# Kernel tuning notes

Measured on AMD Instinct MI355X. Metric: run time of the kernel, lower is better.

Reference implementation:

```python
import jax, jax.numpy as jnp
import numpy as np

K = 16  # neighbors
EPS = 1e-3  # Keras BatchNormalization default epsilon


def _bn(x, gamma, beta, mean, var):
    return (x - mean) * jax.lax.rsqrt(var + EPS) * gamma + beta


def setup_inputs() -> dict:
    key = jax.random.key(0)
    ks = jax.random.split(key, 16)
    B, P, C = 128, 256, 64
    inp = {
        "points": jax.random.normal(ks[0], (B, P, 3), jnp.float32),
        "features": jax.random.normal(ks[1], (B, P, C), jnp.float32),
        "w0": jax.random.normal(ks[2], (2 * C, 64), jnp.float32) * 0.08,
        "w1": jax.random.normal(ks[3], (64, 64), jnp.float32) * 0.12,
        "w2": jax.random.normal(ks[4], (64, 64), jnp.float32) * 0.12,
        "gammas": 0.8 + 0.4 * jax.random.uniform(ks[5], (3, 64), jnp.float32),
        "betas": 0.1 * jax.random.normal(ks[6], (3, 64), jnp.float32),
        "means": 0.1 * jax.random.normal(ks[7], (3, 64), jnp.float32),
        "variances": 0.5 + jax.random.uniform(ks[8], (3, 64), jnp.float32),
        "sc_w": jax.random.normal(ks[9], (C, 64), jnp.float32) * 0.12,
        "sc_gamma": 0.8 + 0.4 * jax.random.uniform(ks[10], (64,), jnp.float32),
        "sc_beta": 0.1 * jax.random.normal(ks[11], (64,), jnp.float32),
        "sc_mean": 0.1 * jax.random.normal(ks[12], (64,), jnp.float32),
        "sc_var": 0.5 + jax.random.uniform(ks[13], (64,), jnp.float32),
    }
    return inp


def reference(points, features, w0, w1, w2, gammas, betas, means, variances,
              sc_w, sc_gamma, sc_beta, sc_mean, sc_var):
    B, P, C = features.shape
    # pairwise squared-distance matrix: ||a||^2 - 2 a.b + ||b||^2  -> [B, P, P]
    r = jnp.sum(points * points, axis=2, keepdims=True)  # [B, P, 1]
    m = jnp.einsum('bpc,bqc->bpq', points, points)
    d = r - 2.0 * m + jnp.swapaxes(r, 1, 2)
    # top_k of -d: K+1 nearest (incl. self at position 0), drop self
    _, idx = jax.lax.top_k(-d, K + 1)
    idx = idx[:, :, 1:]  # [B, P, K]
    # KNN gather of features
    knn_fts = features[jnp.arange(B)[:, None, None], idx]  # [B, P, K, C]
    center = jnp.broadcast_to(features[:, :, None, :], (B, P, K, C))
    x = jnp.concatenate([center, knn_fts - center], axis=-1)  # [B, P, K, 2C]
    # per-edge MLP: 1x1 conv + BN (inference) + relu
    for i, w in enumerate((w0, w1, w2)):
        x = jnp.einsum('bpkc,cd->bpkd', x, w)
        x = _bn(x, gammas[i], betas[i], means[i], variances[i])
        x = jax.nn.relu(x)
    fts = jnp.mean(x, axis=2)  # average pooling over neighbors -> [B, P, 64]
    # shortcut 1x1 conv + BN
    sc = jnp.einsum('bpc,cd->bpd', features, sc_w)
    sc = _bn(sc, sc_gamma, sc_beta, sc_mean, sc_var)
    return jax.nn.relu(sc + fts)
```

## Files before the change

### kernel.cpp

```cpp
#include <hip/hip_runtime.h>
#include <math.h>

#define NBATCH 128
#define NP 256
#define NC 64
#define KNN 16
#define EPSV 1e-3f

typedef __bf16 bf16_t;
typedef bf16_t bf16x8 __attribute__((ext_vector_type(8)));
typedef float f32x4 __attribute__((ext_vector_type(4)));
typedef unsigned short u16x4 __attribute__((ext_vector_type(4)));

static __device__ __forceinline__ f32x4 mfma16(bf16x8 a, bf16x8 b, f32x4 c) {
    return __builtin_amdgcn_mfma_f32_16x16x32_bf16(a, b, c, 0, 0, 0);
}
static __device__ __forceinline__ unsigned short f2bfu(float f) {
    union { bf16_t b; unsigned short u; } cv; cv.b = (bf16_t)f; return cv.u;
}
static __device__ __forceinline__ float bfu2f(unsigned short u) {
    unsigned x = ((unsigned)u) << 16;
    return __int_as_float((int)x);
}
static __device__ __forceinline__ unsigned umin2(unsigned a, unsigned b) { return a < b ? a : b; }
static __device__ __forceinline__ unsigned umax2(unsigned a, unsigned b) { return a > b ? a : b; }

static __device__ __forceinline__ bf16x8 packrelu(f32x4 a, f32x4 b) {
    bf16x8 r;
    r[0] = (bf16_t)fmaxf(a[0], 0.f); r[1] = (bf16_t)fmaxf(a[1], 0.f);
    r[2] = (bf16_t)fmaxf(a[2], 0.f); r[3] = (bf16_t)fmaxf(a[3], 0.f);
    r[4] = (bf16_t)fmaxf(b[0], 0.f); r[5] = (bf16_t)fmaxf(b[1], 0.f);
    r[6] = (bf16_t)fmaxf(b[2], 0.f); r[7] = (bf16_t)fmaxf(b[3], 0.f);
    return r;
}

template <int CTRL>
static __device__ __forceinline__ float dppadd(float v) {
    int x = __builtin_amdgcn_mov_dpp(__float_as_int(v), CTRL, 0xF, 0xF, true);
    return v + __int_as_float(x);
}
static __device__ __forceinline__ float sum16(float v) {
    v = dppadd<0xB1>(v);
    v = dppadd<0x4E>(v);
    v = dppadd<0x141>(v);
    v = dppadd<0x140>(v);
    return v;
}

#define CFENCE() asm volatile("" ::: "memory")

#define INSERTK(k_)                                                   \
    do {                                                              \
        _Pragma("unroll")                                             \
        for (int ii = KNN - 1; ii >= 1; --ii)                         \
            bk[ii] = umin2(umax2((k_), bk[ii - 1]), bk[ii]);          \
        bk[0] = umin2((k_), bk[0]);                                   \
    } while (0)

__global__ __launch_bounds__(256) void prep_kernel(
    const float* __restrict__ w0, const float* __restrict__ w1,
    const float* __restrict__ w2, const float* __restrict__ sc_w,
    const float* __restrict__ gammas, const float* __restrict__ betas,
    const float* __restrict__ means, const float* __restrict__ variances,
    const float* __restrict__ sc_gamma, const float* __restrict__ sc_beta,
    const float* __restrict__ sc_mean, const float* __restrict__ sc_var,
    unsigned short* __restrict__ wsf, float* __restrict__ bnp)
{
    const int tid = blockIdx.x * 256 + threadIdx.x;
    if (tid < 20480) {
        const int region = tid >> 12;
        const int e2 = tid & 4095;
        const int f = e2 >> 9;
        const int r = e2 & 511;
        const int lane = r >> 3, j = r & 7;
        const int ks = f >> 2, t = f & 3;
        const int m = lane & 15;
        const int k_in = ks * 32 + (lane >> 4) * 8 + j;
        const int kp = (t >> 1) * 32 + (m >> 2) * 8 + (t & 1) * 4 + (m & 3);
        float v;
        if (region == 0)      v = w0[k_in * 64 + kp] - w0[(64 + k_in) * 64 + kp];
        else if (region == 1) v = w0[(64 + k_in) * 64 + kp];
        else if (region == 2) {
            float s1 = gammas[k_in] * rsqrtf(variances[k_in] + EPSV);
            v = s1 * w1[k_in * 64 + kp];
        } else if (region == 3) {
            float s2 = gammas[64 + k_in] * rsqrtf(variances[64 + k_in] + EPSV);
            v = s2 * w2[k_in * 64 + kp];
        } else {
            v = sc_w[k_in * 64 + (4 * m + t)];
        }
        wsf[tid] = f2bfu(v);
    } else {
        const int e = tid - 20480;
        if (e < 192) {
            const int L = e >> 6;
            const int pos = e & 63;
            const int t = pos >> 4, m = pos & 15;
            const int c = (t >> 1) * 32 + (m >> 2) * 8 + (t & 1) * 4 + (m & 3);
            float scl = gammas[L * 64 + c] * rsqrtf(variances[L * 64 + c] + EPSV);
            float shf = betas[L * 64 + c] - means[L * 64 + c] * scl;
            bnp[e] = shf / scl;
        } else if (e < 256) {
            const int c = e - 192;
            float s3 = gammas[128 + c] * rsqrtf(variances[128 + c] + EPSV);
            bnp[e] = s3 * (1.f / 16.f);
        } else if (e < 320) {
            const int c = e - 256;
            bnp[e] = sc_gamma[c] * rsqrtf(sc_var[c] + EPSV);
        } else if (e < 384) {
            const int c = e - 320;
            float s = sc_gamma[c] * rsqrtf(sc_var[c] + EPSV);
            bnp[e] = sc_beta[c] - sc_mean[c] * s;
        }
    }
}

__global__ __launch_bounds__(256) void mega_kernel(
    const float* __restrict__ points, const float* __restrict__ features,
    const unsigned short* __restrict__ wsf, const float* __restrict__ bnp,
    float* __restrict__ out)
{
    __shared__ __align__(16) unsigned short fLDS[NP * NC];
    __shared__ __align__(16) float4 sp[NP];
    __shared__ unsigned sk[128][17];
    __shared__ unsigned short nkbuf[128][16];
    __shared__ __align__(16) float s0buf[4][8][64];
    __shared__ __align__(16) unsigned short ftsbuf[4][8][64];

    const int kb = blockIdx.x;
    const int bb = kb >> 1;
    const int qbase = (kb & 1) * 128;
    const int t = threadIdx.x;

    {
        const float* pb = points + (size_t)bb * NP * 3;
        sp[t] = make_float4(pb[t * 3 + 0], pb[t * 3 + 1], pb[t * 3 + 2], 0.f);
        const float* fb = features + (size_t)bb * NP * NC;
#pragma unroll
        for (int cc = 0; cc < 8; ++cc) {
            const int c = t + cc * 256;
            const int row = c >> 3, ch8 = c & 7;
            const float4 a = *(const float4*)&fb[row * NC + ch8 * 8];
            const float4 b2 = *(const float4*)&fb[row * NC + ch8 * 8 + 4];
            union { unsigned short s[8]; uint4 v; } r;
            r.s[0] = f2bfu(a.x); r.s[1] = f2bfu(a.y); r.s[2] = f2bfu(a.z); r.s[3] = f2bfu(a.w);
            r.s[4] = f2bfu(b2.x); r.s[5] = f2bfu(b2.y); r.s[6] = f2bfu(b2.z); r.s[7] = f2bfu(b2.w);
            const int sc = ch8 ^ (row & 7);
            *(uint4*)&fLDS[row * NC + sc * 8] = r.v;
        }
    }
    __syncthreads();

    {
        const int qt = t & 127;
        const int half = t >> 7;
        const int p = qbase + qt;
        const float4 qp = sp[p];
        unsigned bk[KNN];
#pragma unroll
        for (int ii = 0; ii < KNN; ++ii) bk[ii] = 0xFFFFFFFFu;
        const int cbase = half * 128;
#pragma unroll 4
        for (int c = 0; c < 128; ++c) {
            const int cand = cbase + c;
            const float4 P = sp[cand];
            const float dx = qp.x - P.x, dy = qp.y - P.y, dz = qp.z - P.z;
            const float d = fmaf(dx, dx, fmaf(dy, dy, dz * dz));
            unsigned key = (__float_as_uint(d) & 0xFFFFFF00u) | (unsigned)cand;
            key = (cand == p) ? 0xFFFFFFFFu : key;
            INSERTK(key);
        }
        if (half == 1) {
#pragma unroll
            for (int ii = 0; ii < KNN; ++ii) sk[qt][ii] = bk[ii];
        }
        __syncthreads();
        if (half == 0) {
            for (int j = 0; j < KNN; ++j) {
                const unsigned key = sk[qt][j];
                if (key >= bk[KNN - 1]) break;
                INSERTK(key);
            }
#pragma unroll
            for (int ii = 0; ii < KNN; ++ii)
                nkbuf[qt][ii] = (unsigned short)(bk[ii] & 0xFFu);
        }
    }
    __syncthreads();

    const int wid = t >> 6;
    const int l = t & 63;
    const int i = l & 15;
    const int h = l >> 4;

    bf16x8 wr[24];
    {
        const bf16x8* __restrict__ W = (const bf16x8*)(wsf + 4096);
#pragma unroll
        for (int f = 0; f < 24; ++f) wr[f] = W[f * 64 + l];
    }
    f32x4 cin2[4], cin3[4];
#pragma unroll
    for (int tq = 0; tq < 4; ++tq) {
        cin2[tq] = *(const f32x4*)&bnp[64 + tq * 16 + 4 * h];
        cin3[tq] = *(const f32x4*)&bnp[128 + tq * 16 + 4 * h];
    }

    const bf16x8* __restrict__ WV = (const bf16x8*)(wsf);
    const bf16x8* __restrict__ WS = (const bf16x8*)(wsf + 16384);

    for (int seg = 0; seg < 4; ++seg) {
        const int qr0 = seg * 32 + wid * 8;

        {
            const int crow = qbase + qr0 + (i & 7);
            const int swl = crow & 7;
            bf16x8 b0 = *(const bf16x8*)&fLDS[crow * NC + (h ^ swl) * 8];
            bf16x8 b1 = *(const bf16x8*)&fLDS[crow * NC + ((4 + h) ^ swl) * 8];
#pragma unroll
            for (int tq = 0; tq < 4; ++tq) {
                f32x4 acc = *(const f32x4*)&bnp[tq * 16 + 4 * h];
                acc = mfma16(WV[tq * 64 + l], b0, acc);
                acc = mfma16(WV[(4 + tq) * 64 + l], b1, acc);
                if (i < 8)
                    *(f32x4*)&s0buf[wid][i][tq * 16 + 4 * h] = acc;
            }
        }
        int nks[8];
#pragma unroll
        for (int q = 0; q < 8; ++q) nks[q] = nkbuf[qr0 + q][i];
        CFENCE();

        bf16x8 fb0, fb1;
        {
            const int nk = nks[0], swn = nk & 7;
            fb0 = *(const bf16x8*)&fLDS[nk * NC + (h ^ swn) * 8];
            fb1 = *(const bf16x8*)&fLDS[nk * NC + ((4 + h) ^ swn) * 8];
        }

#pragma unroll
        for (int q = 0; q < 8; ++q) {
            f32x4 acc[4];
#pragma unroll
            for (int tq = 0; tq < 4; ++tq) {
                f32x4 z = *(const f32x4*)&s0buf[wid][q][tq * 16 + 4 * h];
                z = mfma16(wr[tq], fb0, z);
                acc[tq] = mfma16(wr[4 + tq], fb1, z);
            }
            bf16x8 g0, g1;
            if (q < 7) {
                const int nk = nks[q + 1], swn = nk & 7;
                g0 = *(const bf16x8*)&fLDS[nk * NC + (h ^ swn) * 8];
                g1 = *(const bf16x8*)&fLDS[nk * NC + ((4 + h) ^ swn) * 8];
            }
            bf16x8 x0 = packrelu(acc[0], acc[1]);
            bf16x8 x1 = packrelu(acc[2], acc[3]);
#pragma unroll
            for (int tq = 0; tq < 4; ++tq) {
                f32x4 z = mfma16(wr[8 + tq], x0, cin2[tq]);
                acc[tq] = mfma16(wr[12 + tq], x1, z);
            }
            bf16x8 y0 = packrelu(acc[0], acc[1]);
            bf16x8 y1 = packrelu(acc[2], acc[3]);
#pragma unroll
            for (int tq = 0; tq < 4; ++tq) {
                f32x4 z = mfma16(wr[16 + tq], y0, cin3[tq]);
                acc[tq] = mfma16(wr[20 + tq], y1, z);
            }
            float st[4][4];
#pragma unroll
            for (int tq = 0; tq < 4; ++tq)
#pragma unroll
                for (int r = 0; r < 4; ++r)
                    st[tq][r] = sum16(fmaxf(acc[tq][r], 0.f));
            if (i == 0) {
#pragma unroll
                for (int tq = 0; tq < 4; ++tq) {
                    u16x4 pk;
#pragma unroll
                    for (int r = 0; r < 4; ++r) pk[r] = f2bfu(st[tq][r]);
                    *(u16x4*)&ftsbuf[wid][q][(tq >> 1) * 32 + h * 8 + (tq & 1) * 4] = pk;
                }
            }
            fb0 = g0; fb1 = g1;
        }
        CFENCE();

        {
            const int i4 = 4 * i;
            float4 sscl = *(const float4*)&bnp[256 + i4];
            float4 sshf = *(const float4*)&bnp[320 + i4];
            float4 f3q  = *(const float4*)&bnp[192 + i4];
            const int crow = qbase + qr0 + (i & 7);
            const int swl = crow & 7;
            bf16x8 a0 = *(const bf16x8*)&fLDS[crow * NC + (h ^ swl) * 8];
            bf16x8 a1 = *(const bf16x8*)&fLDS[crow * NC + ((4 + h) ^ swl) * 8];
            f32x4 acc[4];
#pragma unroll
            for (int tq = 0; tq < 4; ++tq) {
                f32x4 z = {0.f, 0.f, 0.f, 0.f};
                z = mfma16(a0, WS[tq * 64 + l], z);
                acc[tq] = mfma16(a1, WS[(4 + tq) * 64 + l], z);
            }
            if (h < 2) {
                const float* ss_ = (const float*)&sscl;
                const float* sf_ = (const float*)&sshf;
                const float* f3_ = (const float*)&f3q;
#pragma unroll
                for (int r = 0; r < 4; ++r) {
                    const int q = h * 4 + r;
                    u16x4 ftsu = *(const u16x4*)&ftsbuf[wid][q][i4];
                    float4 o;
                    float* o_ = (float*)&o;
#pragma unroll
                    for (int tq = 0; tq < 4; ++tq)
                        o_[tq] = fmaxf(fmaf(acc[tq][r], ss_[tq], sf_[tq]) + bfu2f(ftsu[tq]) * f3_[tq], 0.f);
                    *(float4*)&out[(size_t)(bb * NP + qbase + qr0 + q) * NC + i4] = o;
                }
            }
        }
        CFENCE();
    }
}

extern "C" void kernel_launch(void* const* d_in, const int* in_sizes, int n_in,
                              void* d_out, int out_size, void* d_ws, size_t ws_size,
                              hipStream_t stream) {
    const float* points    = (const float*)d_in[0];
    const float* features  = (const float*)d_in[1];
    const float* w0        = (const float*)d_in[2];
    const float* w1        = (const float*)d_in[3];
    const float* w2        = (const float*)d_in[4];
    const float* gammas    = (const float*)d_in[5];
    const float* betas     = (const float*)d_in[6];
    const float* means     = (const float*)d_in[7];
    const float* variances = (const float*)d_in[8];
    const float* sc_w      = (const float*)d_in[9];
    const float* sc_gamma  = (const float*)d_in[10];
    const float* sc_beta   = (const float*)d_in[11];
    const float* sc_mean   = (const float*)d_in[12];
    const float* sc_var    = (const float*)d_in[13];
    float* out = (float*)d_out;

    unsigned short* wsf = (unsigned short*)d_ws;
    float* bnp = (float*)((char*)d_ws + 40960);

    prep_kernel<<<82, 256, 0, stream>>>(w0, w1, w2, sc_w, gammas, betas, means,
                                        variances, sc_gamma, sc_beta, sc_mean,
                                        sc_var, wsf, bnp);
    mega_kernel<<<NBATCH * 2, 256, 0, stream>>>(points, features, wsf, bnp, out);
}
```

Measured before the change: 51.80 us.

## Split work into 32-query blocks with tree KNN merge and direct global gathers

Result: slower. 54.76 us (+5.7%).

```diff
diff --git a/kernel.cpp b/kernel.cpp
--- a/kernel.cpp
+++ b/kernel.cpp
@@ -25,6 +25,12 @@
 static __device__ __forceinline__ unsigned umin2(unsigned a, unsigned b) { return a < b ? a : b; }
 static __device__ __forceinline__ unsigned umax2(unsigned a, unsigned b) { return a > b ? a : b; }
 
+static __device__ __forceinline__ bf16x8 pack8(float4 a, float4 b) {
+    bf16x8 r;
+    r[0] = (bf16_t)a.x; r[1] = (bf16_t)a.y; r[2] = (bf16_t)a.z; r[3] = (bf16_t)a.w;
+    r[4] = (bf16_t)b.x; r[5] = (bf16_t)b.y; r[6] = (bf16_t)b.z; r[7] = (bf16_t)b.w;
+    return r;
+}
 static __device__ __forceinline__ bf16x8 packrelu(f32x4 a, f32x4 b) {
     bf16x8 r;
     r[0] = (bf16_t)fmaxf(a[0], 0.f); r[1] = (bf16_t)fmaxf(a[1], 0.f);
@@ -115,53 +121,41 @@
     }
 }
 
-__global__ __launch_bounds__(256) void mega_kernel(
+__global__ __launch_bounds__(256) void knedge_kernel(
     const float* __restrict__ points, const float* __restrict__ features,
     const unsigned short* __restrict__ wsf, const float* __restrict__ bnp,
     float* __restrict__ out)
 {
-    __shared__ __align__(16) unsigned short fLDS[NP * NC];
     __shared__ __align__(16) float4 sp[NP];
-    __shared__ unsigned sk[128][17];
-    __shared__ unsigned short nkbuf[128][16];
+    __shared__ unsigned mrg[32][4][17];
+    __shared__ unsigned short nkbuf[32][16];
     __shared__ __align__(16) float s0buf[4][8][64];
     __shared__ __align__(16) unsigned short ftsbuf[4][8][64];
-
-    const int kb = blockIdx.x;
-    const int bb = kb >> 1;
-    const int qbase = (kb & 1) * 128;
+    __shared__ __align__(16) float cinlds[128];
+
+    const int kb = (blockIdx.x & 7) * 128 + (blockIdx.x >> 3);
+    const int bb = kb >> 3;
+    const int q0 = (kb & 7) * 32;
     const int t = threadIdx.x;
 
     {
         const float* pb = points + (size_t)bb * NP * 3;
         sp[t] = make_float4(pb[t * 3 + 0], pb[t * 3 + 1], pb[t * 3 + 2], 0.f);
-        const float* fb = features + (size_t)bb * NP * NC;
-#pragma unroll
-        for (int cc = 0; cc < 8; ++cc) {
-            const int c = t + cc * 256;
-            const int row = c >> 3, ch8 = c & 7;
-            const float4 a = *(const float4*)&fb[row * NC + ch8 * 8];
-            const float4 b2 = *(const float4*)&fb[row * NC + ch8 * 8 + 4];
-            union { unsigned short s[8]; uint4 v; } r;
-            r.s[0] = f2bfu(a.x); r.s[1] = f2bfu(a.y); r.s[2] = f2bfu(a.z); r.s[3] = f2bfu(a.w);
-            r.s[4] = f2bfu(b2.x); r.s[5] = f2bfu(b2.y); r.s[6] = f2bfu(b2.z); r.s[7] = f2bfu(b2.w);
-            const int sc = ch8 ^ (row & 7);
-            *(uint4*)&fLDS[row * NC + sc * 8] = r.v;
-        }
+        if (t < 128) cinlds[t] = bnp[64 + t];
     }
     __syncthreads();
 
     {
-        const int qt = t & 127;
-        const int half = t >> 7;
-        const int p = qbase + qt;
+        const int q = t & 31;
+        const int oct = t >> 5;
+        const int p = q0 + q;
         const float4 qp = sp[p];
         unsigned bk[KNN];
 #pragma unroll
         for (int ii = 0; ii < KNN; ++ii) bk[ii] = 0xFFFFFFFFu;
-        const int cbase = half * 128;
+        const int cbase = oct * 32;
 #pragma unroll 4
-        for (int c = 0; c < 128; ++c) {
+        for (int c = 0; c < 32; ++c) {
             const int cand = cbase + c;
             const float4 P = sp[cand];
             const float dx = qp.x - P.x, dy = qp.y - P.y, dz = qp.z - P.z;
@@ -170,20 +164,49 @@
             key = (cand == p) ? 0xFFFFFFFFu : key;
             INSERTK(key);
         }
-        if (half == 1) {
-#pragma unroll
-            for (int ii = 0; ii < KNN; ++ii) sk[qt][ii] = bk[ii];
-        }
-        __syncthreads();
-        if (half == 0) {
+        if (oct & 1) {
+#pragma unroll
+            for (int ii = 0; ii < KNN; ++ii) mrg[q][oct >> 1][ii] = bk[ii];
+        }
+        __syncthreads();
+        if (!(oct & 1)) {
+            const unsigned* src = mrg[q][oct >> 1];
             for (int j = 0; j < KNN; ++j) {
-                const unsigned key = sk[qt][j];
+                const unsigned key = src[j];
                 if (key >= bk[KNN - 1]) break;
                 INSERTK(key);
             }
+        }
+        __syncthreads();
+        if (oct == 2 || oct == 6) {
+#pragma unroll
+            for (int ii = 0; ii < KNN; ++ii) mrg[q][oct >> 2][ii] = bk[ii];
+        }
+        __syncthreads();
+        if (oct == 0 || oct == 4) {
+            const unsigned* src = mrg[q][oct >> 2];
+            for (int j = 0; j < KNN; ++j) {
+                const unsigned key = src[j];
+                if (key >= bk[KNN - 1]) break;
+                INSERTK(key);
+            }
+        }
+        __syncthreads();
+        if (oct == 4) {
+#pragma unroll
+            for (int ii = 0; ii < KNN; ++ii) mrg[q][0][ii] = bk[ii];
+        }
+        __syncthreads();
+        if (oct == 0) {
+            const unsigned* src = mrg[q][0];
+            for (int j = 0; j < KNN; ++j) {
+                const unsigned key = src[j];
+                if (key >= bk[KNN - 1]) break;
+                INSERTK(key);
+            }
 #pragma unroll
             for (int ii = 0; ii < KNN; ++ii)
-                nkbuf[qt][ii] = (unsigned short)(bk[ii] & 0xFFu);
+                nkbuf[q][ii] = (unsigned short)(bk[ii] & 0xFFu);
         }
     }
     __syncthreads();
@@ -192,6 +215,7 @@
     const int l = t & 63;
     const int i = l & 15;
     const int h = l >> 4;
+    const int prel = q0 + wid * 8;
 
     bf16x8 wr[24];
     {
@@ -199,127 +223,125 @@
 #pragma unroll
         for (int f = 0; f < 24; ++f) wr[f] = W[f * 64 + l];
     }
-    f32x4 cin2[4], cin3[4];
-#pragma unroll
-    for (int tq = 0; tq < 4; ++tq) {
-        cin2[tq] = *(const f32x4*)&bnp[64 + tq * 16 + 4 * h];
-        cin3[tq] = *(const f32x4*)&bnp[128 + tq * 16 + 4 * h];
-    }
-
     const bf16x8* __restrict__ WV = (const bf16x8*)(wsf);
     const bf16x8* __restrict__ WS = (const bf16x8*)(wsf + 16384);
-
-    for (int seg = 0; seg < 4; ++seg) {
-        const int qr0 = seg * 32 + wid * 8;
-
-        {
-            const int crow = qbase + qr0 + (i & 7);
-            const int swl = crow & 7;
-            bf16x8 b0 = *(const bf16x8*)&fLDS[crow * NC + (h ^ swl) * 8];
-            bf16x8 b1 = *(const bf16x8*)&fLDS[crow * NC + ((4 + h) ^ swl) * 8];
+    const float* __restrict__ fbat = features + (size_t)bb * NP * NC;
+
+    bf16x8 a0, a1;
+    {
+        const float* cp = fbat + (size_t)(prel + (i & 7)) * NC;
+        float4 c0 = *(const float4*)(cp + 8 * h);
+        float4 c1 = *(const float4*)(cp + 8 * h + 4);
+        float4 c2 = *(const float4*)(cp + 32 + 8 * h);
+        float4 c3 = *(const float4*)(cp + 32 + 8 * h + 4);
+        a0 = pack8(c0, c1);
+        a1 = pack8(c2, c3);
+    }
+
+#pragma unroll
+    for (int tq = 0; tq < 4; ++tq) {
+        f32x4 acc = *(const f32x4*)&bnp[tq * 16 + 4 * h];
+        acc = mfma16(WV[tq * 64 + l], a0, acc);
+        acc = mfma16(WV[(4 + tq) * 64 + l], a1, acc);
+        if (i < 8)
+            *(f32x4*)&s0buf[wid][i][tq * 16 + 4 * h] = acc;
+    }
+    int nks[8];
+#pragma unroll
+    for (int q = 0; q < 8; ++q) nks[q] = nkbuf[wid * 8 + q][i];
+    CFENCE();
+
+    bf16x8 fb0, fb1;
+    {
+        const float* np_ = fbat + (size_t)nks[0] * NC;
+        float4 n0 = *(const float4*)(np_ + 8 * h);
+        float4 n1 = *(const float4*)(np_ + 8 * h + 4);
+        float4 n2 = *(const float4*)(np_ + 32 + 8 * h);
+        float4 n3 = *(const float4*)(np_ + 32 + 8 * h + 4);
+        fb0 = pack8(n0, n1);
+        fb1 = pack8(n2, n3);
+    }
+
+#pragma unroll
+    for (int q = 0; q < 8; ++q) {
+        f32x4 acc[4];
+#pragma unroll
+        for (int tq = 0; tq < 4; ++tq) {
+            f32x4 z = *(const f32x4*)&s0buf[wid][q][tq * 16 + 4 * h];
+            z = mfma16(wr[tq], fb0, z);
+            acc[tq] = mfma16(wr[4 + tq], fb1, z);
+        }
+        bf16x8 g0, g1;
+        if (q < 7) {
+            const float* np_ = fbat + (size_t)nks[q + 1] * NC;
+            float4 n0 = *(const float4*)(np_ + 8 * h);
+            float4 n1 = *(const float4*)(np_ + 8 * h + 4);
+            float4 n2 = *(const float4*)(np_ + 32 + 8 * h);
+            float4 n3 = *(const float4*)(np_ + 32 + 8 * h + 4);
+            g0 = pack8(n0, n1);
+            g1 = pack8(n2, n3);
+        }
+        bf16x8 x0 = packrelu(acc[0], acc[1]);
+        bf16x8 x1 = packrelu(acc[2], acc[3]);
+#pragma unroll
+        for (int tq = 0; tq < 4; ++tq) {
+            f32x4 z = mfma16(wr[8 + tq], x0, *(const f32x4*)&cinlds[tq * 16 + 4 * h]);
+            acc[tq] = mfma16(wr[12 + tq], x1, z);
+        }
+        bf16x8 y0 = packrelu(acc[0], acc[1]);
+        bf16x8 y1 = packrelu(acc[2], acc[3]);
+#pragma unroll
+        for (int tq = 0; tq < 4; ++tq) {
+            f32x4 z = mfma16(wr[16 + tq], y0, *(const f32x4*)&cinlds[64 + tq * 16 + 4 * h]);
+            acc[tq] = mfma16(wr[20 + tq], y1, z);
+        }
+        float st[4][4];
+#pragma unroll
+        for (int tq = 0; tq < 4; ++tq)
+#pragma unroll
+            for (int r = 0; r < 4; ++r)
+                st[tq][r] = sum16(fmaxf(acc[tq][r], 0.f));
+        if (i == 0) {
 #pragma unroll
             for (int tq = 0; tq < 4; ++tq) {
-                f32x4 acc = *(const f32x4*)&bnp[tq * 16 + 4 * h];
-                acc = mfma16(WV[tq * 64 + l], b0, acc);
-                acc = mfma16(WV[(4 + tq) * 64 + l], b1, acc);
-                if (i < 8)
-                    *(f32x4*)&s0buf[wid][i][tq * 16 + 4 * h] = acc;
-            }
-        }
-        int nks[8];
-#pragma unroll
-        for (int q = 0; q < 8; ++q) nks[q] = nkbuf[qr0 + q][i];
-        CFENCE();
-
-        bf16x8 fb0, fb1;
-        {
-            const int nk = nks[0], swn = nk & 7;
-            fb0 = *(const bf16x8*)&fLDS[nk * NC + (h ^ swn) * 8];
-            fb1 = *(const bf16x8*)&fLDS[nk * NC + ((4 + h) ^ swn) * 8];
-        }
-
-#pragma unroll
-        for (int q = 0; q < 8; ++q) {
-            f32x4 acc[4];
-#pragma unroll
-            for (int tq = 0; tq < 4; ++tq) {
-                f32x4 z = *(const f32x4*)&s0buf[wid][q][tq * 16 + 4 * h];
-                z = mfma16(wr[tq], fb0, z);
-                acc[tq] = mfma16(wr[4 + tq], fb1, z);
-            }
-            bf16x8 g0, g1;
-            if (q < 7) {
-                const int nk = nks[q + 1], swn = nk & 7;
-                g0 = *(const bf16x8*)&fLDS[nk * NC + (h ^ swn) * 8];
-                g1 = *(const bf16x8*)&fLDS[nk * NC + ((4 + h) ^ swn) * 8];
-            }
-            bf16x8 x0 = packrelu(acc[0], acc[1]);
-            bf16x8 x1 = packrelu(acc[2], acc[3]);
-#pragma unroll
-            for (int tq = 0; tq < 4; ++tq) {
-                f32x4 z = mfma16(wr[8 + tq], x0, cin2[tq]);
-                acc[tq] = mfma16(wr[12 + tq], x1, z);
-            }
-            bf16x8 y0 = packrelu(acc[0], acc[1]);
-            bf16x8 y1 = packrelu(acc[2], acc[3]);
-#pragma unroll
-            for (int tq = 0; tq < 4; ++tq) {
-                f32x4 z = mfma16(wr[16 + tq], y0, cin3[tq]);
-                acc[tq] = mfma16(wr[20 + tq], y1, z);
-            }
-            float st[4][4];
-#pragma unroll
-            for (int tq = 0; tq < 4; ++tq)
-#pragma unroll
-                for (int r = 0; r < 4; ++r)
-                    st[tq][r] = sum16(fmaxf(acc[tq][r], 0.f));
-            if (i == 0) {
-#pragma unroll
-                for (int tq = 0; tq < 4; ++tq) {
-                    u16x4 pk;
-#pragma unroll
-                    for (int r = 0; r < 4; ++r) pk[r] = f2bfu(st[tq][r]);
-                    *(u16x4*)&ftsbuf[wid][q][(tq >> 1) * 32 + h * 8 + (tq & 1) * 4] = pk;
-                }
-            }
-            fb0 = g0; fb1 = g1;
-        }
-        CFENCE();
-
-        {
-            const int i4 = 4 * i;
-            float4 sscl = *(const float4*)&bnp[256 + i4];
-            float4 sshf = *(const float4*)&bnp[320 + i4];
-            float4 f3q  = *(const float4*)&bnp[192 + i4];
-            const int crow = qbase + qr0 + (i & 7);
-            const int swl = crow & 7;
-            bf16x8 a0 = *(const bf16x8*)&fLDS[crow * NC + (h ^ swl) * 8];
-            bf16x8 a1 = *(const bf16x8*)&fLDS[crow * NC + ((4 + h) ^ swl) * 8];
-            f32x4 acc[4];
-#pragma unroll
-            for (int tq = 0; tq < 4; ++tq) {
-                f32x4 z = {0.f, 0.f, 0.f, 0.f};
-                z = mfma16(a0, WS[tq * 64 + l], z);
-                acc[tq] = mfma16(a1, WS[(4 + tq) * 64 + l], z);
-            }
-            if (h < 2) {
-                const float* ss_ = (const float*)&sscl;
-                const float* sf_ = (const float*)&sshf;
-                const float* f3_ = (const float*)&f3q;
-#pragma unroll
-                for (int r = 0; r < 4; ++r) {
-                    const int q = h * 4 + r;
-                    u16x4 ftsu = *(const u16x4*)&ftsbuf[wid][q][i4];
-                    float4 o;
-                    float* o_ = (float*)&o;
-#pragma unroll
-                    for (int tq = 0; tq < 4; ++tq)
-                        o_[tq] = fmaxf(fmaf(acc[tq][r], ss_[tq], sf_[tq]) + bfu2f(ftsu[tq]) * f3_[tq], 0.f);
-                    *(float4*)&out[(size_t)(bb * NP + qbase + qr0 + q) * NC + i4] = o;
-                }
-            }
-        }
-        CFENCE();
+                u16x4 pk;
+#pragma unroll
+                for (int r = 0; r < 4; ++r) pk[r] = f2bfu(st[tq][r]);
+                *(u16x4*)&ftsbuf[wid][q][(tq >> 1) * 32 + h * 8 + (tq & 1) * 4] = pk;
+            }
+        }
+        fb0 = g0; fb1 = g1;
+    }
+    CFENCE();
+
+    {
+        const int i4 = 4 * i;
+        float4 sscl = *(const float4*)&bnp[256 + i4];
+        float4 sshf = *(const float4*)&bnp[320 + i4];
+        float4 f3q  = *(const float4*)&bnp[192 + i4];
+        f32x4 acc[4];
+#pragma unroll
+        for (int tq = 0; tq < 4; ++tq) {
+            f32x4 z = {0.f, 0.f, 0.f, 0.f};
+            z = mfma16(a0, WS[tq * 64 + l], z);
+            acc[tq] = mfma16(a1, WS[(4 + tq) * 64 + l], z);
+        }
+        if (h < 2) {
+            const float* ss_ = (const float*)&sscl;
+            const float* sf_ = (const float*)&sshf;
+            const float* f3_ = (const float*)&f3q;
+#pragma unroll
+            for (int r = 0; r < 4; ++r) {
+                const int q = h * 4 + r;
+                u16x4 ftsu = *(const u16x4*)&ftsbuf[wid][q][i4];
+                float4 o;
+                float* o_ = (float*)&o;
+#pragma unroll
+                for (int tq = 0; tq < 4; ++tq)
+                    o_[tq] = fmaxf(fmaf(acc[tq][r], ss_[tq], sf_[tq]) + bfu2f(ftsu[tq]) * f3_[tq], 0.f);
+                *(float4*)&out[(size_t)(bb * NP + prel + q) * NC + i4] = o;
+            }
+        }
     }
 }
 
@@ -348,5 +370,5 @@
     prep_kernel<<<82, 256, 0, stream>>>(w0, w1, w2, sc_w, gammas, betas, means,
                                         variances, sc_gamma, sc_beta, sc_mean,
                                         sc_var, wsf, bnp);
-    mega_kernel<<<NBATCH * 2, 256, 0, stream>>>(points, features, wsf, bnp, out);
-}
+    knedge_kernel<<<NBATCH * 8, 256, 0, stream>>>(points, features, wsf, bnp, out);
+}
```
